# Kernel optimization log

Measured on AMD Instinct MI355X. Metric: run time of the kernel, lower is better.

## Reference

```python
import jax, jax.numpy as jnp
import numpy as np

B, C, N, E, F = 8, 4, 2048, 512, 2048
EPS = 1e-5
MASK_SCALE = 5.0


def layer_norm(x, gamma, beta):
    mu = jnp.mean(x, axis=-1, keepdims=True)
    var = jnp.mean(jnp.square(x - mu), axis=-1, keepdims=True)
    return (x - mu) * jax.lax.rsqrt(var + EPS) * gamma + beta


def setup_inputs() -> dict:
    key = jax.random.key(0)
    ks = jax.random.split(key, 8)
    src = jax.random.normal(ks[0], (B, C, N, E), dtype=jnp.float32)
    key_padding_mask = jax.random.uniform(ks[1], (B, N), dtype=jnp.float32)
    # FFN params (torch Linear default init scale ~ U(-1/sqrt(fan_in), +))
    W1 = jax.random.normal(ks[2], (E, F), dtype=jnp.float32) / np.sqrt(E)
    b1 = jnp.zeros((F,), dtype=jnp.float32)
    W2 = jax.random.normal(ks[3], (F, E), dtype=jnp.float32) / np.sqrt(F)
    b2 = jnp.zeros((E,), dtype=jnp.float32)
    g1 = jnp.ones((E,), dtype=jnp.float32)
    be1 = jnp.zeros((E,), dtype=jnp.float32)
    g2 = jnp.ones((E,), dtype=jnp.float32)
    be2 = jnp.zeros((E,), dtype=jnp.float32)
    return {"src": src, "key_padding_mask": key_padding_mask,
            "W1": W1, "b1": b1, "W2": W2, "b2": b2,
            "g1": g1, "be1": be1, "g2": g2, "be2": be2}


def reference(src, key_padding_mask, W1, b1, W2, b2, g1, be1, g2, be2):
    # src: [B, C, N, E]; channels batched into one fused attention call
    scale = 1.0 / jnp.sqrt(jnp.asarray(src.shape[-1], src.dtype))
    scores = jnp.einsum('bcne,bcme->bcnm', src, src) * scale  # [B,C,N,N]
    scores = scores - key_padding_mask[:, None, None, :] * MASK_SCALE
    attn = jax.nn.softmax(scores, axis=-1)
    attn_out = jnp.einsum('bcnm,bcme->bcne', attn, src)
    # residual + norm1 (dropout is identity at eval)
    src2 = layer_norm(src + attn_out, g1, be1)
    # feedforward: Linear -> ReLU -> Linear
    ff = jax.nn.relu(jnp.einsum('bcne,ef->bcnf', src2, W1) + b1)
    ff = jnp.einsum('bcnf,fe->bcne', ff, W2) + b2
    out = layer_norm(src2 + ff, g2, be2)
    return out
```

## Files before the change

kernel.cpp:

```cpp
#include <hip/hip_runtime.h>
#include <stdint.h>

constexpr int CB = 8, CC = 4, CN = 2048, CE = 512, CF = 2048;
constexpr long long TOT = (long long)CB * CC * CN * CE;
constexpr int GRP = 16;
constexpr int MCH = 65536;
constexpr float SCALE = 0.04419417382415922f;
constexpr float MASK_SCALE = 5.0f;
constexpr float EPS = 1e-5f;

typedef unsigned short bf16_t;
typedef __attribute__((ext_vector_type(4))) float f32x4;
typedef __attribute__((ext_vector_type(8))) short s16x8;

#define DEV static __device__ __forceinline__

DEV unsigned short f2bf(float f) {
    unsigned u = __float_as_uint(f);
    unsigned r = (u + 0x7fffu + ((u >> 16) & 1u)) >> 16;
    return (unsigned short)r;
}
DEV float bf2f(unsigned short b) {
    return __uint_as_float(((unsigned)b) << 16);
}

typedef const __attribute__((address_space(1))) unsigned int* gptr_t;
typedef __attribute__((address_space(3))) unsigned int* lptr_t;
DEV void async16(const void* g, void* l) {
    __builtin_amdgcn_global_load_lds((gptr_t)g, (lptr_t)l, 16, 0, 0);
}

#define FULL_BAR() do { asm volatile("" ::: "memory"); __builtin_amdgcn_s_barrier(); asm volatile("" ::: "memory"); } while (0)
#define LGKM0() asm volatile("s_waitcnt lgkmcnt(0)" ::: "memory")
#define LGKM8() asm volatile("s_waitcnt lgkmcnt(8)" ::: "memory")
#define SCHED0() __builtin_amdgcn_sched_barrier(0)
#define VMCNT(N_) asm volatile("s_waitcnt vmcnt(" #N_ ")" ::: "memory")

DEV float blockSum256(float v, float* sm) {
    #pragma unroll
    for (int o = 32; o; o >>= 1) v += __shfl_xor(v, o);
    int w = threadIdx.x >> 6;
    __syncthreads();
    if ((threadIdx.x & 63) == 0) sm[w] = v;
    __syncthreads();
    return sm[0] + sm[1] + sm[2] + sm[3];
}
DEV float blockMax256(float v, float* sm) {
    #pragma unroll
    for (int o = 32; o; o >>= 1) v = fmaxf(v, __shfl_xor(v, o));
    int w = threadIdx.x >> 6;
    __syncthreads();
    if ((threadIdx.x & 63) == 0) sm[w] = v;
    __syncthreads();
    return fmaxf(fmaxf(sm[0], sm[1]), fmaxf(sm[2], sm[3]));
}

__global__ __launch_bounds__(256) void cvt_f32_bf16_vec(
    const float* __restrict__ in, bf16_t* __restrict__ out, long long n) {
    long long i = ((long long)blockIdx.x * 256 + threadIdx.x) * 4;
    long long stride = (long long)gridDim.x * 1024;
    for (; i < n; i += stride) {
        float4 v = *reinterpret_cast<const float4*>(in + i);
        ushort4 u;
        u.x = f2bf(v.x); u.y = f2bf(v.y); u.z = f2bf(v.z); u.w = f2bf(v.w);
        *reinterpret_cast<ushort4*>(out + i) = u;
    }
}

__global__ __launch_bounds__(256) void transpose_f32_bf16(
    const float* __restrict__ in, bf16_t* __restrict__ out,
    int R, int Cc) {
    __shared__ float tile[32][33];
    int rb = blockIdx.y * 32, cb = blockIdx.x * 32;
    int tx = threadIdx.x & 31, ty = threadIdx.x >> 5;
    #pragma unroll
    for (int i = 0; i < 32; i += 8)
        tile[ty + i][tx] = in[(size_t)(rb + ty + i) * Cc + cb + tx];
    __syncthreads();
    #pragma unroll
    for (int i = 0; i < 32; i += 8)
        out[(size_t)(cb + ty + i) * R + rb + tx] = f2bf(tile[tx][ty + i]);
}

__global__ __launch_bounds__(256) void transpose_bf16(
    const bf16_t* __restrict__ in, bf16_t* __restrict__ out,
    int R, int Cc, long long sIn, long long sOut) {
    __shared__ bf16_t tile[32][36];
    const bf16_t* inz = in + (size_t)blockIdx.z * sIn;
    bf16_t* outz = out + (size_t)blockIdx.z * sOut;
    int rb = blockIdx.y * 32, cb = blockIdx.x * 32;
    int t = threadIdx.x;
    int r = t >> 3, c4 = (t & 7) * 4;
    *(ushort4*)&tile[r][c4] = *(const ushort4*)&inz[(size_t)(rb + r) * Cc + cb + c4];
    __syncthreads();
    int c = t >> 3, r4 = (t & 7) * 4;
    ushort4 w;
    w.x = tile[r4 + 0][c]; w.y = tile[r4 + 1][c];
    w.z = tile[r4 + 2][c]; w.w = tile[r4 + 3][c];
    *(ushort4*)&outz[(size_t)(cb + c) * R + rb + r4] = w;
}

template <int EPI>
__global__ __launch_bounds__(512, 2) void gemm256(
    const bf16_t* __restrict__ A, const bf16_t* __restrict__ B,
    void* __restrict__ Cptr, const float* __restrict__ bias, float alpha,
    int Nc, int K, long long sA, long long sB, long long sC) {
    extern __shared__ bf16_t lds[];
    bf16_t* AsL = lds;
    bf16_t* BsL = lds + 32768;

    int bx, by, bz;
    {
        int gx = gridDim.x, gy = gridDim.y;
        int nwg = gx * gy * gridDim.z;
        int flat = blockIdx.x + gx * (blockIdx.y + gy * blockIdx.z);
        int wg = (nwg & 7) ? flat : ((flat & 7) * (nwg >> 3) + (flat >> 3));
        bx = wg % gx;
        int tmp = wg / gx;
        by = tmp % gy;
        bz = tmp / gy;
    }

    const bf16_t* Az = A + (size_t)bz * sA;
    const bf16_t* Bz = B + (size_t)bz * sB;
    const int t = threadIdx.x;
    const int lane = t & 63, wid = t >> 6;
    const int wr = wid >> 2, wc = wid & 3;
    const int brow = by * 256, bcol = bx * 256;
    const int NT = K >> 6;

    const int r0 = t >> 3, s0 = t & 7;
    const int ce = ((s0 ^ (r0 & 7)) << 3);
    const bf16_t* aP0 = Az + (size_t)(brow + r0) * K + ce;
    const bf16_t* bP0 = Bz + (size_t)(bcol + r0) * K + ce;
    const size_t rK64 = (size_t)64 * K;
    const size_t h128K = rK64 * 2;

    #define PUSH_A(kt_, h_) do { \
        bf16_t* d_ = AsL + ((((kt_) & 1) * 2 + (h_)) * 8192); \
        const bf16_t* s_ = aP0 + (size_t)(h_) * h128K + (size_t)(kt_) * 64; \
        async16(s_, d_ + t * 8); \
        async16(s_ + rK64, d_ + 4096 + t * 8); \
    } while (0)
    #define PUSH_B(kt_, h_) do { \
        bf16_t* d_ = BsL + ((((kt_) & 1) * 2 + (h_)) * 8192); \
        const bf16_t* s_ = bP0 + (size_t)(h_) * h128K + (size_t)(kt_) * 64; \
        async16(s_, d_ + t * 8); \
        async16(s_ + rK64, d_ + 4096 + t * 8); \
    } while (0)

    const int q = lane >> 4, rr0 = lane & 15, xmask = rr0 & 7;
    s16x8 af[4][2];
    s16x8 bv[2][2][2];
    f32x4 acc[2][2][4][2] = {};

    #define READ_A(ktp_, qm_) do { \
        const bf16_t* base_ = AsL + (((ktp_) * 2 + (qm_)) * 8192); \
        _Pragma("unroll") for (int m_ = 0; m_ < 4; ++m_) \
        _Pragma("unroll") for (int ks_ = 0; ks_ < 2; ++ks_) \
            af[m_][ks_] = *(const s16x8*)(base_ + (wr * 64 + m_ * 16 + rr0) * 64 + (((ks_ * 4 + q) ^ xmask) << 3)); \
    } while (0)
    #define READ_B(ktp_, qn_) do { \
        const bf16_t* base_ = BsL + (((ktp_) * 2 + (qn_)) * 8192); \
        _Pragma("unroll") for (int n_ = 0; n_ < 2; ++n_) \
        _Pragma("unroll") for (int ks_ = 0; ks_ < 2; ++ks_) \
            bv[qn_][n_][ks_] = *(const s16x8*)(base_ + (wc * 32 + n_ * 16 + rr0) * 64 + (((ks_ * 4 + q) ^ xmask) << 3)); \
    } while (0)
    #define MFMA_Q(qm_, qn_) do { \
        __builtin_amdgcn_s_setprio(1); \
        _Pragma("unroll") for (int m_ = 0; m_ < 4; ++m_) \
        _Pragma("unroll") for (int n_ = 0; n_ < 2; ++n_) \
        _Pragma("unroll") for (int ks_ = 0; ks_ < 2; ++ks_) \
            acc[qm_][qn_][m_][n_] = __builtin_amdgcn_mfma_f32_16x16x32_bf16( \
                af[m_][ks_], bv[qn_][n_][ks_], acc[qm_][qn_][m_][n_], 0, 0, 0); \
        __builtin_amdgcn_s_setprio(0); \
    } while (0)

    PUSH_A(0, 0); PUSH_B(0, 0); PUSH_B(0, 1); PUSH_A(0, 1);
    VMCNT(4);
    PUSH_A(1, 0); PUSH_B(1, 0); PUSH_B(1, 1);
    VMCNT(6);
    FULL_BAR();

    for (int T = 0; T < NT; ++T) {
        const int p = T & 1;
        const bool m1 = (T + 1 < NT), m2 = (T + 2 < NT);
        READ_A(p, 0);
        READ_B(p, 0);
        if (m1) PUSH_A(T + 1, 1);
        LGKM8();
        FULL_BAR(); LGKM0(); SCHED0();
        MFMA_Q(0, 0);
        FULL_BAR();
        READ_B(p, 1);
        if (m2) PUSH_A(T + 2, 0);
        FULL_BAR(); LGKM0(); SCHED0();
        MFMA_Q(0, 1);
        FULL_BAR();
        READ_A(p, 1);
        if (m2) PUSH_B(T + 2, 0);
        FULL_BAR(); LGKM0(); SCHED0();
        MFMA_Q(1, 0);
        FULL_BAR();
        if (m2) { PUSH_B(T + 2, 1); VMCNT(6); } else { VMCNT(0); }
        FULL_BAR();
        MFMA_Q(1, 1);
        FULL_BAR();
    }

    {
        size_t cz = (size_t)bz * sC;
        bf16_t* Cb = (bf16_t*)Cptr + cz;
        const int lo = lane & 1;
        #pragma unroll
        for (int qm = 0; qm < 2; ++qm)
        #pragma unroll
        for (int qn = 0; qn < 2; ++qn)
        #pragma unroll
        for (int n = 0; n < 2; ++n) {
            int col = bcol + qn * 128 + wc * 32 + n * 16 + rr0;
            float bvv = (EPI == 1 || EPI == 4) ? bias[col] : 0.f;
            #pragma unroll
            for (int m = 0; m < 4; ++m) {
                unsigned words[4];
                #pragma unroll
                for (int j = 0; j < 4; ++j) {
                    float v = acc[qm][qn][m][n][j] + bvv;
                    if constexpr (EPI == 1) v = fmaxf(v, 0.f);
                    if constexpr (EPI == 3) v *= alpha;
                    unsigned h = f2bf(v);
                    unsigned o = (unsigned)__shfl_xor((int)h, 1);
                    words[j] = lo ? (o | (h << 16)) : (h | (o << 16));
                }
                int row = brow + qm * 128 + wr * 64 + m * 16 + q * 4 + lo * 2;
                int cp = col & ~1;
                *(unsigned*)&Cb[(size_t)row * Nc + cp] = words[lo * 2];
                *(unsigned*)&Cb[(size_t)(row + 1) * Nc + cp] = words[lo * 2 + 1];
            }
        }
    }
    #undef PUSH_A
    #undef PUSH_B
    #undef READ_A
    #undef READ_B
    #undef MFMA_Q
}

__global__ __launch_bounds__(256) void softmax_bf16(
    bf16_t* __restrict__ S, const float* __restrict__ mask, int bc0) {
    __shared__ float sm[4];
    int gr = blockIdx.x;
    int b = (bc0 + (gr >> 11)) >> 2;
    bf16_t* row = S + (size_t)gr * CN;
    int tid = threadIdx.x;
    const float* mrow = mask + (size_t)b * CN + tid * 8;
    s16x8 v = *(const s16x8*)(row + tid * 8);
    float4 m0 = *(const float4*)(mrow);
    float4 m1 = *(const float4*)(mrow + 4);
    float x[8];
    x[0] = bf2f((unsigned short)v[0]) - m0.x * MASK_SCALE;
    x[1] = bf2f((unsigned short)v[1]) - m0.y * MASK_SCALE;
    x[2] = bf2f((unsigned short)v[2]) - m0.z * MASK_SCALE;
    x[3] = bf2f((unsigned short)v[3]) - m0.w * MASK_SCALE;
    x[4] = bf2f((unsigned short)v[4]) - m1.x * MASK_SCALE;
    x[5] = bf2f((unsigned short)v[5]) - m1.y * MASK_SCALE;
    x[6] = bf2f((unsigned short)v[6]) - m1.z * MASK_SCALE;
    x[7] = bf2f((unsigned short)v[7]) - m1.w * MASK_SCALE;
    float mx = -3.4e38f;
    #pragma unroll
    for (int i = 0; i < 8; i++) mx = fmaxf(mx, x[i]);
    mx = blockMax256(mx, sm);
    float s = 0.f;
    #pragma unroll
    for (int i = 0; i < 8; i++) { x[i] = __expf(x[i] - mx); s += x[i]; }
    s = blockSum256(s, sm);
    float inv = 1.f / s;
    s16x8 u;
    #pragma unroll
    for (int i = 0; i < 8; i++) u[i] = (short)f2bf(x[i] * inv);
    *(s16x8*)(row + tid * 8) = u;
}

__global__ __launch_bounds__(256) void ln1_kernel(
    const bf16_t* __restrict__ src, const bf16_t* __restrict__ ao,
    const float* __restrict__ g, const float* __restrict__ be,
    bf16_t* __restrict__ o) {
    __shared__ float sm[4];
    size_t base = (size_t)blockIdx.x * CE;
    int e = threadIdx.x * 2;
    ushort2 s = *(const ushort2*)&src[base + e];
    ushort2 a = *(const ushort2*)&ao[base + e];
    float x0 = bf2f(s.x) + bf2f(a.x), x1 = bf2f(s.y) + bf2f(a.y);
    float mu = blockSum256(x0 + x1, sm) * (1.f / CE);
    float d0 = x0 - mu, d1 = x1 - mu;
    float var = blockSum256(d0 * d0 + d1 * d1, sm) * (1.f / CE);
    float rs = rsqrtf(var + EPS);
    ushort2 w;
    w.x = f2bf(d0 * rs * g[e] + be[e]);
    w.y = f2bf(d1 * rs * g[e + 1] + be[e + 1]);
    *(ushort2*)&o[base + e] = w;
}

__global__ __launch_bounds__(256) void ln2_kernel(
    const bf16_t* __restrict__ a, const bf16_t* __restrict__ b,
    const float* __restrict__ g, const float* __restrict__ be,
    float* __restrict__ o) {
    __shared__ float sm[4];
    size_t base = (size_t)blockIdx.x * CE;
    int e = threadIdx.x * 2;
    ushort2 aa = *(const ushort2*)&a[base + e];
    ushort2 bb = *(const ushort2*)&b[base + e];
    float x0 = bf2f(aa.x) + bf2f(bb.x), x1 = bf2f(aa.y) + bf2f(bb.y);
    float mu = blockSum256(x0 + x1, sm) * (1.f / CE);
    float d0 = x0 - mu, d1 = x1 - mu;
    float var = blockSum256(d0 * d0 + d1 * d1, sm) * (1.f / CE);
    float rs = rsqrtf(var + EPS);
    float2 w;
    w.x = d0 * rs * g[e] + be[e];
    w.y = d1 * rs * g[e + 1] + be[e + 1];
    *(float2*)&o[base + e] = w;
}

extern "C" void kernel_launch(void* const* d_in, const int* in_sizes, int n_in,
                              void* d_out, int out_size, void* d_ws, size_t ws_size,
                              hipStream_t stream) {
    const float* src  = (const float*)d_in[0];
    const float* mask = (const float*)d_in[1];
    const float* W1   = (const float*)d_in[2];
    const float* b1   = (const float*)d_in[3];
    const float* W2   = (const float*)d_in[4];
    const float* b2   = (const float*)d_in[5];
    const float* g1   = (const float*)d_in[6];
    const float* be1  = (const float*)d_in[7];
    const float* g2   = (const float*)d_in[8];
    const float* be2  = (const float*)d_in[9];
    float* out = (float*)d_out;
    char* ws = (char*)d_ws;

    hipFuncSetAttribute(reinterpret_cast<const void*>(&gemm256<1>), hipFuncAttributeMaxDynamicSharedMemorySize, 131072);
    hipFuncSetAttribute(reinterpret_cast<const void*>(&gemm256<3>), hipFuncAttributeMaxDynamicSharedMemorySize, 131072);
    hipFuncSetAttribute(reinterpret_cast<const void*>(&gemm256<4>), hipFuncAttributeMaxDynamicSharedMemorySize, 131072);

    const size_t MB = 1024 * 1024;
    bf16_t* probs  = (bf16_t*)(ws);
    bf16_t* src_bf = (bf16_t*)(ws + 256 * MB);
    bf16_t* srcT   = (bf16_t*)(ws + 320 * MB);
    bf16_t* attnO  = (bf16_t*)(ws + 384 * MB);
    bf16_t* W1T    = (bf16_t*)(ws + 448 * MB);
    bf16_t* W2T    = (bf16_t*)(ws + 450 * MB);
    bf16_t* src2   = (bf16_t*)(ws);
    bf16_t* ff     = (bf16_t*)(ws + 64 * MB);
    bf16_t* H      = (bf16_t*)(ws + 128 * MB);
    if (ws_size < 452 * MB) return;

    cvt_f32_bf16_vec<<<4096, 256, 0, stream>>>(src, src_bf, TOT);
    transpose_f32_bf16<<<dim3(CF / 32, CE / 32, 1), 256, 0, stream>>>(W1, W1T, CE, CF);
    transpose_f32_bf16<<<dim3(CE / 32, CF / 32, 1), 256, 0, stream>>>(W2, W2T, CF, CE);
    transpose_bf16<<<dim3(CE / 32, CN / 32, 32), 256, 0, stream>>>(
        src_bf, srcT, CN, CE, (long long)CN * CE, (long long)CE * CN);

    for (int g0 = 0; g0 < CB * CC; g0 += GRP) {
        const bf16_t* srcb = src_bf + (size_t)g0 * CN * CE;
        bf16_t* probs_g = probs + (size_t)g0 * CN * CN;
        gemm256<3><<<dim3(CN / 256, CN / 256, GRP), 512, 131072, stream>>>(
            srcb, srcb, probs_g, nullptr, SCALE, CN, CE,
            (long long)CN * CE, (long long)CN * CE, (long long)CN * CN);
        softmax_bf16<<<dim3(GRP * CN), 256, 0, stream>>>(probs_g, mask, g0);
        gemm256<3><<<dim3(CE / 256, CN / 256, GRP), 512, 131072, stream>>>(
            probs_g, srcT + (size_t)g0 * CE * CN, attnO + (size_t)g0 * CN * CE,
            nullptr, 1.0f, CE, CN,
            (long long)CN * CN, (long long)CE * CN, (long long)CN * CE);
    }
    ln1_kernel<<<dim3(CB * CC * CN), 256, 0, stream>>>(src_bf, attnO, g1, be1, src2);

    gemm256<1><<<dim3(CF / 256, MCH / 256, 1), 512, 131072, stream>>>(
        src2, W1T, H, b1, 1.0f, CF, CE, 0, 0, 0);
    gemm256<4><<<dim3(CE / 256, MCH / 256, 1), 512, 131072, stream>>>(
        H, W2T, ff, b2, 1.0f, CE, CF, 0, 0, 0);
    ln2_kernel<<<dim3(MCH), 256, 0, stream>>>(src2, ff, g2, be2, out);
}
```

Before: 903.3 us.

## Add 128x128 single-buffered GEMM for short-K matmuls and fuse cvt with transpose

Adds a smaller 128x128-tile GEMM kernel with 256 threads, static LDS and no double buffering. It is used for the two GEMMs with K=512 (the QK^T score GEMM and the first FFN GEMM), with the aim of better occupancy and a cheaper prologue than the 256x256 kernel. Separately, the f32-to-bf16 conversion of src is fused with the transpose that produces srcT, so the bf16 copy is no longer re-read. In exchange, the new GEMM loses the deeper pipelining and larger reuse of the 256-tile kernel, and its LDS fragment reads may cause bank conflicts.

After: 946.5 us. 1.05x slower.

```diff
diff --git a/kernel.cpp b/kernel.cpp
--- a/kernel.cpp
+++ b/kernel.cpp
@@ -55,16 +55,27 @@
     return fmaxf(fmaxf(sm[0], sm[1]), fmaxf(sm[2], sm[3]));
 }
 
-__global__ __launch_bounds__(256) void cvt_f32_bf16_vec(
-    const float* __restrict__ in, bf16_t* __restrict__ out, long long n) {
-    long long i = ((long long)blockIdx.x * 256 + threadIdx.x) * 4;
-    long long stride = (long long)gridDim.x * 1024;
-    for (; i < n; i += stride) {
-        float4 v = *reinterpret_cast<const float4*>(in + i);
-        ushort4 u;
-        u.x = f2bf(v.x); u.y = f2bf(v.y); u.z = f2bf(v.z); u.w = f2bf(v.w);
-        *reinterpret_cast<ushort4*>(out + i) = u;
-    }
+__global__ __launch_bounds__(256) void cvt_transpose(
+    const float* __restrict__ in, bf16_t* __restrict__ outN,
+    bf16_t* __restrict__ outT) {
+    __shared__ bf16_t tile[32][33];
+    const float* inz = in + (size_t)blockIdx.z * CN * CE;
+    bf16_t* oN = outN + (size_t)blockIdx.z * CN * CE;
+    bf16_t* oT = outT + (size_t)blockIdx.z * CE * CN;
+    int rb = blockIdx.y * 32;
+    int cb = blockIdx.x * 32;
+    int tx = threadIdx.x & 31, ty = threadIdx.x >> 5;
+    #pragma unroll
+    for (int i = 0; i < 32; i += 8) {
+        float v = inz[(size_t)(rb + ty + i) * CE + cb + tx];
+        unsigned short h = f2bf(v);
+        oN[(size_t)(rb + ty + i) * CE + cb + tx] = h;
+        tile[ty + i][tx] = h;
+    }
+    __syncthreads();
+    #pragma unroll
+    for (int i = 0; i < 32; i += 8)
+        oT[(size_t)(cb + ty + i) * CN + rb + tx] = tile[tx][ty + i];
 }
 
 __global__ __launch_bounds__(256) void transpose_f32_bf16(
@@ -82,22 +93,74 @@
         out[(size_t)(cb + ty + i) * R + rb + tx] = f2bf(tile[tx][ty + i]);
 }
 
-__global__ __launch_bounds__(256) void transpose_bf16(
-    const bf16_t* __restrict__ in, bf16_t* __restrict__ out,
-    int R, int Cc, long long sIn, long long sOut) {
-    __shared__ bf16_t tile[32][36];
-    const bf16_t* inz = in + (size_t)blockIdx.z * sIn;
-    bf16_t* outz = out + (size_t)blockIdx.z * sOut;
-    int rb = blockIdx.y * 32, cb = blockIdx.x * 32;
-    int t = threadIdx.x;
-    int r = t >> 3, c4 = (t & 7) * 4;
-    *(ushort4*)&tile[r][c4] = *(const ushort4*)&inz[(size_t)(rb + r) * Cc + cb + c4];
-    __syncthreads();
-    int c = t >> 3, r4 = (t & 7) * 4;
-    ushort4 w;
-    w.x = tile[r4 + 0][c]; w.y = tile[r4 + 1][c];
-    w.z = tile[r4 + 2][c]; w.w = tile[r4 + 3][c];
-    *(ushort4*)&outz[(size_t)(cb + c) * R + rb + r4] = w;
+template <int EPI>
+__global__ __launch_bounds__(256, 4) void gemm_bt(
+    const bf16_t* __restrict__ A, const bf16_t* __restrict__ B,
+    void* __restrict__ Cptr, const float* __restrict__ bias, float alpha,
+    int Nc, int K, long long sA, long long sB, long long sC) {
+    __shared__ bf16_t As[128 * 32];
+    __shared__ bf16_t Bs[128 * 32];
+    const bf16_t* Az = A + (size_t)blockIdx.z * sA;
+    const bf16_t* Bz = B + (size_t)blockIdx.z * sB;
+    int tid = threadIdx.x;
+    int lane = tid & 63, wid = tid >> 6;
+    int wr = wid >> 1, wc = wid & 1;
+    int brow = blockIdx.y * 128, bcol = blockIdx.x * 128;
+
+    f32x4 acc[4][4] = {};
+
+    int c0 = tid, c1 = tid + 256;
+    const bf16_t* Ag0 = Az + (size_t)(brow + (c0 >> 2)) * K + (c0 & 3) * 8;
+    const bf16_t* Ag1 = Az + (size_t)(brow + (c1 >> 2)) * K + (c1 & 3) * 8;
+    const bf16_t* Bg0 = Bz + (size_t)(bcol + (c0 >> 2)) * K + (c0 & 3) * 8;
+    const bf16_t* Bg1 = Bz + (size_t)(bcol + (c1 >> 2)) * K + (c1 & 3) * 8;
+
+    for (int k0 = 0; k0 < K; k0 += 32) {
+        async16(Ag0 + k0, &As[c0 * 8]);
+        async16(Ag1 + k0, &As[c1 * 8]);
+        async16(Bg0 + k0, &Bs[c0 * 8]);
+        async16(Bg1 + k0, &Bs[c1 * 8]);
+        __syncthreads();
+        s16x8 af[4], bv[4];
+        #pragma unroll
+        for (int m = 0; m < 4; m++)
+            af[m] = *(const s16x8*)&As[(wr * 64 + m * 16 + (lane & 15)) * 32 + (lane >> 4) * 8];
+        #pragma unroll
+        for (int n = 0; n < 4; n++)
+            bv[n] = *(const s16x8*)&Bs[(wc * 64 + n * 16 + (lane & 15)) * 32 + (lane >> 4) * 8];
+        #pragma unroll
+        for (int m = 0; m < 4; m++)
+            #pragma unroll
+            for (int n = 0; n < 4; n++)
+                acc[m][n] = __builtin_amdgcn_mfma_f32_16x16x32_bf16(af[m], bv[n], acc[m][n], 0, 0, 0);
+        __syncthreads();
+    }
+
+    size_t cz = (size_t)blockIdx.z * sC;
+    bf16_t* Cb = (bf16_t*)Cptr + cz;
+    const int q = lane >> 4, rr0 = lane & 15, lo = lane & 1;
+    #pragma unroll
+    for (int m = 0; m < 4; m++) {
+        #pragma unroll
+        for (int n = 0; n < 4; n++) {
+            int col = bcol + wc * 64 + n * 16 + rr0;
+            float bvv = (EPI == 1 || EPI == 4) ? bias[col] : 0.f;
+            unsigned words[4];
+            #pragma unroll
+            for (int j = 0; j < 4; j++) {
+                float v = acc[m][n][j] + bvv;
+                if constexpr (EPI == 1) v = fmaxf(v, 0.f);
+                if constexpr (EPI == 3) v *= alpha;
+                unsigned h = f2bf(v);
+                unsigned o = (unsigned)__shfl_xor((int)h, 1);
+                words[j] = lo ? (o | (h << 16)) : (h | (o << 16));
+            }
+            int row = brow + wr * 64 + m * 16 + q * 4 + lo * 2;
+            int cp = col & ~1;
+            *(unsigned*)&Cb[(size_t)row * Nc + cp] = words[lo * 2];
+            *(unsigned*)&Cb[(size_t)(row + 1) * Nc + cp] = words[lo * 2 + 1];
+        }
+    }
 }
 
 template <int EPI>
@@ -337,7 +400,6 @@
     float* out = (float*)d_out;
     char* ws = (char*)d_ws;
 
-    hipFuncSetAttribute(reinterpret_cast<const void*>(&gemm256<1>), hipFuncAttributeMaxDynamicSharedMemorySize, 131072);
     hipFuncSetAttribute(reinterpret_cast<const void*>(&gemm256<3>), hipFuncAttributeMaxDynamicSharedMemorySize, 131072);
     hipFuncSetAttribute(reinterpret_cast<const void*>(&gemm256<4>), hipFuncAttributeMaxDynamicSharedMemorySize, 131072);
 
@@ -353,16 +415,14 @@
     bf16_t* H      = (bf16_t*)(ws + 128 * MB);
     if (ws_size < 452 * MB) return;
 
-    cvt_f32_bf16_vec<<<4096, 256, 0, stream>>>(src, src_bf, TOT);
+    cvt_transpose<<<dim3(CE / 32, CN / 32, 32), 256, 0, stream>>>(src, src_bf, srcT);
     transpose_f32_bf16<<<dim3(CF / 32, CE / 32, 1), 256, 0, stream>>>(W1, W1T, CE, CF);
     transpose_f32_bf16<<<dim3(CE / 32, CF / 32, 1), 256, 0, stream>>>(W2, W2T, CF, CE);
-    transpose_bf16<<<dim3(CE / 32, CN / 32, 32), 256, 0, stream>>>(
-        src_bf, srcT, CN, CE, (long long)CN * CE, (long long)CE * CN);
 
     for (int g0 = 0; g0 < CB * CC; g0 += GRP) {
         const bf16_t* srcb = src_bf + (size_t)g0 * CN * CE;
         bf16_t* probs_g = probs + (size_t)g0 * CN * CN;
-        gemm256<3><<<dim3(CN / 256, CN / 256, GRP), 512, 131072, stream>>>(
+        gemm_bt<3><<<dim3(CN / 128, CN / 128, GRP), 256, 0, stream>>>(
             srcb, srcb, probs_g, nullptr, SCALE, CN, CE,
             (long long)CN * CE, (long long)CN * CE, (long long)CN * CN);
         softmax_bf16<<<dim3(GRP * CN), 256, 0, stream>>>(probs_g, mask, g0);
@@ -373,7 +433,7 @@
     }
     ln1_kernel<<<dim3(CB * CC * CN), 256, 0, stream>>>(src_bf, attnO, g1, be1, src2);
 
-    gemm256<1><<<dim3(CF / 256, MCH / 256, 1), 512, 131072, stream>>>(
+    gemm_bt<1><<<dim3(CF / 128, MCH / 128, 1), 256, 0, stream>>>(
         src2, W1T, H, b1, 1.0f, CF, CE, 0, 0, 0);
     gemm256<4><<<dim3(CE / 256, MCH / 256, 1), 512, 131072, stream>>>(
         H, W2T, ff, b2, 1.0f, CE, CF, 0, 0, 0);
```
